# Performance work log

Hardware: AMD Instinct MI355X
Metric: run time of the kernel (lower is better)

Reference implementation:

```python
import jax, jax.numpy as jnp
import numpy as np

INPUT_DIM = 512
DEGREE = 3
NUM_KNOTS = 16
NUM_NEURONS = 1024
OUTPUT_DIM = 512
NUM_BASIS = NUM_KNOTS + DEGREE - 1  # 18


def make_knots():
    # uniform grid on [0,1], extended by `degree` knots on each side
    h = 1.0 / (NUM_KNOTS - 1)
    grid = np.linspace(0.0, 1.0, NUM_KNOTS)
    lo = grid[0] - h * np.arange(DEGREE, 0, -1)
    hi = grid[-1] + h * np.arange(1, DEGREE + 1)
    return jnp.asarray(np.concatenate([lo, grid, hi]), dtype=jnp.float32)  # [NUM_KNOTS+2*DEGREE]


def bspline_basis(x, t, degree):
    # x: [B, N]; t: [K] uniform extended knots. Cox-de Boor recursion.
    K = t.shape[0]
    xb = x[..., None]
    B = ((xb >= t[:-1]) & (xb < t[1:])).astype(x.dtype)  # [B, N, K-1]
    for p in range(1, degree + 1):
        ti = t[: K - p - 1]
        tip = t[p : K - 1]
        ti1 = t[1 : K - p]
        tip1 = t[p + 1 : K]
        left = (xb - ti) / (tip - ti) * B[..., :-1]
        right = (tip1 - xb) / (tip1 - ti1) * B[..., 1:]
        B = left + right
    return B  # [B, N, K-1-degree] == [B, N, NUM_BASIS]


def norm_layer(x, eps=1e-8):
    # per-row min-max normalization into the spline domain [0,1)
    mn = jnp.min(x, axis=-1, keepdims=True)
    mx = jnp.max(x, axis=-1, keepdims=True)
    return (x - mn) / (mx - mn + eps)


def setup_inputs() -> dict:
    key = jax.random.key(0)
    ks = jax.random.split(key, 7)
    x = jax.random.normal(ks[0], (4096, INPUT_DIM), dtype=jnp.float32)
    s1 = 1.0 / np.sqrt(INPUT_DIM)
    s2 = 1.0 / np.sqrt(NUM_NEURONS)
    W1 = jax.random.uniform(ks[1], (INPUT_DIM, NUM_NEURONS), jnp.float32, -s1, s1)
    b1 = jax.random.uniform(ks[2], (NUM_NEURONS,), jnp.float32, -s1, s1)
    coeff = jax.random.normal(ks[3], (NUM_NEURONS, NUM_BASIS), dtype=jnp.float32) * 0.1
    sp_bias = jnp.zeros((NUM_NEURONS,), dtype=jnp.float32)
    W2 = jax.random.uniform(ks[4], (NUM_NEURONS, OUTPUT_DIM), jnp.float32, -s2, s2)
    b2 = jax.random.uniform(ks[5], (OUTPUT_DIM,), jnp.float32, -s2, s2)
    return {"x": x, "W1": W1, "b1": b1, "coeff": coeff, "sp_bias": sp_bias, "W2": W2, "b2": b2}


def reference(x, W1, b1, coeff, sp_bias, W2, b2):
    t = make_knots()
    h = x @ W1 + b1                      # [B, N]  Linear 1
    h = norm_layer(h)                    # NormLayer -> [0,1)
    basis = bspline_basis(h, t, DEGREE)  # [B, N, NUM_BASIS]
    sp = jnp.einsum('bnk,nk->bn', basis, coeff) + sp_bias  # per-neuron spline eval
    out = sp @ W2 + b2                   # Linear 2
    return jax.nn.relu(out)
```

## Files before the change

### kernel.cpp

```cpp
#include <hip/hip_runtime.h>

#define M_ROWS  4096
#define IN_DIM  512
#define NEURONS 1024
#define OUT_DIM 512

typedef _Float16 f16;
typedef __attribute__((ext_vector_type(8))) _Float16 f16x8;
typedef __attribute__((ext_vector_type(4))) _Float16 f16x4;
typedef __attribute__((ext_vector_type(4))) float    f32x4;

__global__ __launch_bounds__(256) void prep(
    const float* __restrict__ x,  f16* __restrict__ xh,
    const float* __restrict__ W1, f16* __restrict__ W1t,
    const float* __restrict__ W2, f16* __restrict__ W2t,
    const float* __restrict__ coeff, const float* __restrict__ spb,
    float* __restrict__ cp)
{
    __shared__ float S[32][33];
    const int b = blockIdx.x, t = threadIdx.x;
    if (b < 1024) {
        int i = b * 256 + t;
        const float4* p = (const float4*)x;
        float4 a = p[i * 2], c = p[i * 2 + 1];
        f16x8 o = { (f16)a.x, (f16)a.y, (f16)a.z, (f16)a.w,
                    (f16)c.x, (f16)c.y, (f16)c.z, (f16)c.w };
        *(f16x8*)(xh + (size_t)i * 8) = o;
        return;
    }
    if (b < 1536) {
        const int tile = b - 1024;
        const int tx = tile & 31, ty = tile >> 5;
        const int tr = t >> 3, tc = (t & 7) * 4;
        float4 v = *(const float4*)&W1[(size_t)(ty * 32 + tr) * NEURONS + tx * 32 + tc];
        S[tr][tc + 0] = v.x; S[tr][tc + 1] = v.y;
        S[tr][tc + 2] = v.z; S[tr][tc + 3] = v.w;
        __syncthreads();
        f16x4 o = {(f16)S[tc + 0][tr], (f16)S[tc + 1][tr],
                   (f16)S[tc + 2][tr], (f16)S[tc + 3][tr]};
        *(f16x4*)&W1t[(size_t)(tx * 32 + tr) * IN_DIM + ty * 32 + tc] = o;
        return;
    }
    if (b < 2048) {
        const int tile = b - 1536;
        const int nt = tile & 15, kt2 = tile >> 4;
        const int tr = t >> 3, tc = (t & 7) * 4;
        float4 v = *(const float4*)&W2[(size_t)(kt2 * 32 + tr) * OUT_DIM + nt * 32 + tc];
        S[tr][tc + 0] = v.x; S[tr][tc + 1] = v.y;
        S[tr][tc + 2] = v.z; S[tr][tc + 3] = v.w;
        __syncthreads();
        f16x4 o = {(f16)S[tc + 0][tr], (f16)S[tc + 1][tr],
                   (f16)S[tc + 2][tr], (f16)S[tc + 3][tr]};
        *(f16x4*)&W2t[(size_t)(nt * 32 + tr) * NEURONS + kt2 * 32 + tc] = o;
        return;
    }
    {
        const int tid = (b - 2048) * 256 + t;
        if (tid < NEURONS * 15) {
            const int n = tid / 15, ii = tid % 15;
            const float s = spb[n];
            float4 c;
            c.x = coeff[n * 18 + ii]     + s;
            c.y = coeff[n * 18 + ii + 1] + s;
            c.z = coeff[n * 18 + ii + 2] + s;
            c.w = coeff[n * 18 + ii + 3] + s;
            *(float4*)&cp[(size_t)tid * 4] = c;
        }
    }
}

__global__ __launch_bounds__(256) void k_gemm1(
    const f16* __restrict__ A, const f16* __restrict__ Bt,
    const float* __restrict__ b1, f16* __restrict__ h,
    float* __restrict__ pmin, float* __restrict__ pmax)
{
    __shared__ f16 lds[2][(128 + 64) * 64];

    const int t    = threadIdx.x;
    const int lane = t & 63, l15 = lane & 15, lhi = lane >> 4;
    const int wid  = t >> 6;
    const int wm   = wid >> 1, wn = wid & 1;

    const int flat = blockIdx.y * gridDim.x + blockIdx.x;
    const int swz  = (flat & 7) * 64 + (flat >> 3);
    const int m0   = (swz >> 4) * 128;
    const int n0   = (swz & 15) * 64;

    auto stage = [&](int buf, int kt) {
        f16* base = &lds[buf][0];
#pragma unroll
        for (int j = 0; j < 4; ++j) {
            int c = wid * 4 + j;
            const f16* g = A + (size_t)(m0 + c * 8 + (lane >> 3)) * IN_DIM + kt + (lane & 7) * 8;
            __builtin_amdgcn_global_load_lds(
                (const __attribute__((address_space(1))) void*)g,
                (__attribute__((address_space(3))) void*)(base + c * 512), 16, 0, 0);
        }
#pragma unroll
        for (int j = 0; j < 2; ++j) {
            int c = wid * 2 + j;
            const f16* g = Bt + (size_t)(n0 + c * 8 + (lane >> 3)) * IN_DIM + kt + (lane & 7) * 8;
            __builtin_amdgcn_global_load_lds(
                (const __attribute__((address_space(1))) void*)g,
                (__attribute__((address_space(3))) void*)(base + 8192 + c * 512), 16, 0, 0);
        }
    };

    f32x4 acc[4][2];
#pragma unroll
    for (int i = 0; i < 4; ++i)
#pragma unroll
        for (int j = 0; j < 2; ++j) acc[i][j] = (f32x4)0.f;

    stage(0, 0);
    __syncthreads();

    int cur = 0;
    for (int tt = 0; tt < 8; ++tt) {
        if (tt < 7) stage(cur ^ 1, (tt + 1) * 64);
        const f16* L = &lds[cur][0];
#pragma unroll
        for (int ks = 0; ks < 2; ++ks) {
            f16x8 bfr[2];
#pragma unroll
            for (int nj = 0; nj < 2; ++nj)
                bfr[nj] = *(const f16x8*)
                    &L[8192 + (wn * 32 + nj * 16 + l15) * 64 + ks * 32 + lhi * 8];
#pragma unroll
            for (int mi = 0; mi < 4; ++mi) {
                f16x8 afr = *(const f16x8*)
                    &L[(wm * 64 + mi * 16 + l15) * 64 + ks * 32 + lhi * 8];
#pragma unroll
                for (int nj = 0; nj < 2; ++nj)
                    acc[mi][nj] = __builtin_amdgcn_mfma_f32_16x16x32_f16(
                        afr, bfr[nj], acc[mi][nj], 0, 0, 0);
            }
        }
        __syncthreads();
        cur ^= 1;
    }

    const int nb2 = (n0 >> 6) * 2 + wn;
#pragma unroll
    for (int mi = 0; mi < 4; ++mi) {
        const int row0 = m0 + wm * 64 + mi * 16 + lhi * 4;
        float vmn[4], vmx[4];
#pragma unroll
        for (int nj = 0; nj < 2; ++nj) {
            const int col = n0 + wn * 32 + nj * 16 + l15;
            const float bv = b1[col];
#pragma unroll
            for (int j = 0; j < 4; ++j) {
                f16 hv = (f16)(acc[mi][nj][j] + bv);
                h[(size_t)(row0 + j) * NEURONS + col] = hv;
                float vr = (float)hv;
                if (nj == 0) { vmn[j] = vr; vmx[j] = vr; }
                else { vmn[j] = fminf(vmn[j], vr); vmx[j] = fmaxf(vmx[j], vr); }
            }
        }
#pragma unroll
        for (int j = 0; j < 4; ++j) {
#pragma unroll
            for (int d = 1; d < 16; d <<= 1) {
                vmn[j] = fminf(vmn[j], __shfl_xor(vmn[j], d));
                vmx[j] = fmaxf(vmx[j], __shfl_xor(vmx[j], d));
            }
        }
        if (l15 == 0) {
#pragma unroll
            for (int j = 0; j < 4; ++j) {
                pmin[(size_t)nb2 * M_ROWS + row0 + j] = vmn[j];
                pmax[(size_t)nb2 * M_ROWS + row0 + j] = vmx[j];
            }
        }
    }
}

__global__ __launch_bounds__(256) void k_spline(
    const f16* __restrict__ h, const float* __restrict__ pmin,
    const float* __restrict__ pmax, const float* __restrict__ cp,
    f16* __restrict__ sph)
{
    const int t    = threadIdx.x;
    const int lane = t & 63;
    const int row  = blockIdx.x * 4 + (t >> 6);

    float mn = pmin[(size_t)(lane & 31) * M_ROWS + row];
    float mx = pmax[(size_t)(lane & 31) * M_ROWS + row];
#pragma unroll
    for (int d = 1; d < 32; d <<= 1) {
        mn = fminf(mn, __shfl_xor(mn, d));
        mx = fmaxf(mx, __shfl_xor(mx, d));
    }
    const float inv = 1.0f / (mx - mn + 1e-8f);

#pragma unroll
    for (int half = 0; half < 2; ++half) {
        const int k0 = half * 512 + lane * 8;
        f16x8 hv = *(const f16x8*)&h[(size_t)row * NEURONS + k0];
        f16x8 o;
#pragma unroll
        for (int e = 0; e < 8; ++e) {
            const float u   = ((float)hv[e] - mn) * inv;
            const float t15 = u * 15.0f;
            int ii = (int)t15;
            ii = ii < 0 ? 0 : (ii > 14 ? 14 : ii);
            const float tl  = t15 - (float)ii;
            const float t2  = tl * tl, t3 = t2 * tl;
            const float omt = 1.0f - tl;
            const float b0  = omt * omt * omt * (1.0f / 6.0f);
            const float b3v = t3 * (1.0f / 6.0f);
            const float b1v = (4.0f / 6.0f) - t2 + 0.5f * t3;
            const float b2v = (1.0f / 6.0f) + 0.5f * (tl + t2 - t3);
            const float4 c  = *(const float4*)&cp[((size_t)(k0 + e) * 15 + ii) * 4];
            o[e] = (f16)(c.x * b0 + c.y * b1v + c.z * b2v + c.w * b3v);
        }
        *(f16x8*)&sph[(size_t)row * NEURONS + k0] = o;
    }
}

__global__ __launch_bounds__(256) void k_gemm2(
    const f16* __restrict__ A, const f16* __restrict__ Bt,
    const float* __restrict__ b2, float* __restrict__ out)
{
    __shared__ f16 lds[2][128 * 128];

    const int t    = threadIdx.x;
    const int lane = t & 63, l15 = lane & 15, lhi = lane >> 4;
    const int wid  = t >> 6;
    const int wm   = wid >> 1, wn = wid & 1;

    const int flat = blockIdx.x;
    const int swz  = (flat & 7) * 64 + (flat >> 3);
    const int m0   = (swz >> 3) * 64;
    const int n0   = (swz & 7) * 64;

    auto stage = [&](int buf, int kt) {
        f16* base = &lds[buf][0];
#pragma unroll
        for (int j = 0; j < 4; ++j) {
            int c = wid * 4 + j;
            const f16* g = A + (size_t)(m0 + c * 4 + (lane >> 4)) * NEURONS + kt + (lane & 15) * 8;
            __builtin_amdgcn_global_load_lds(
                (const __attribute__((address_space(1))) void*)g,
                (__attribute__((address_space(3))) void*)(base + c * 512), 16, 0, 0);
        }
#pragma unroll
        for (int j = 0; j < 4; ++j) {
            int c = wid * 4 + j;
            const f16* g = Bt + (size_t)(n0 + c * 4 + (lane >> 4)) * NEURONS + kt + (lane & 15) * 8;
            __builtin_amdgcn_global_load_lds(
                (const __attribute__((address_space(1))) void*)g,
                (__attribute__((address_space(3))) void*)(base + 8192 + c * 512), 16, 0, 0);
        }
    };

    f32x4 acc[2][2];
#pragma unroll
    for (int i = 0; i < 2; ++i)
#pragma unroll
        for (int j = 0; j < 2; ++j) acc[i][j] = (f32x4)0.f;

    stage(0, 0);
    __syncthreads();

    int cur = 0;
    for (int tt = 0; tt < 8; ++tt) {
        if (tt < 7) stage(cur ^ 1, (tt + 1) * 128);
        const f16* L = &lds[cur][0];
#pragma unroll
        for (int ks = 0; ks < 4; ++ks) {
            f16x8 bfr[2];
#pragma unroll
            for (int nj = 0; nj < 2; ++nj)
                bfr[nj] = *(const f16x8*)
                    &L[8192 + (wn * 32 + nj * 16 + l15) * 128 + ks * 32 + lhi * 8];
#pragma unroll
            for (int mi = 0; mi < 2; ++mi) {
                f16x8 afr = *(const f16x8*)
                    &L[(wm * 32 + mi * 16 + l15) * 128 + ks * 32 + lhi * 8];
#pragma unroll
                for (int nj = 0; nj < 2; ++nj)
                    acc[mi][nj] = __builtin_amdgcn_mfma_f32_16x16x32_f16(
                        afr, bfr[nj], acc[mi][nj], 0, 0, 0);
            }
        }
        __syncthreads();
        cur ^= 1;
    }

#pragma unroll
    for (int mi = 0; mi < 2; ++mi) {
        const int row0 = m0 + wm * 32 + mi * 16 + lhi * 4;
#pragma unroll
        for (int nj = 0; nj < 2; ++nj) {
            const int col = n0 + wn * 32 + nj * 16 + l15;
            const float bv = b2[col];
#pragma unroll
            for (int j = 0; j < 4; ++j)
                out[(size_t)(row0 + j) * OUT_DIM + col] =
                    fmaxf(acc[mi][nj][j] + bv, 0.0f);
        }
    }
}

extern "C" void kernel_launch(void* const* d_in, const int* in_sizes, int n_in,
                              void* d_out, int out_size, void* d_ws, size_t ws_size,
                              hipStream_t stream)
{
    const float* x     = (const float*)d_in[0];
    const float* W1    = (const float*)d_in[1];
    const float* b1    = (const float*)d_in[2];
    const float* coeff = (const float*)d_in[3];
    const float* spb   = (const float*)d_in[4];
    const float* W2    = (const float*)d_in[5];
    const float* b2    = (const float*)d_in[6];
    float* out = (float*)d_out;

    char* ws = (char*)d_ws;
    f16*   h    = (f16*)ws;
    f16*   sph  = (f16*)(ws + ( 8u << 20));
    f16*   xh   = (f16*)(ws + (16u << 20));
    f16*   W1t  = (f16*)(ws + (20u << 20));
    f16*   W2t  = (f16*)(ws + (21u << 20));
    float* pmin = (float*)(ws + (22u << 20));
    float* pmax = (float*)(ws + (22u << 20) + (512u << 10));
    float* cp   = (float*)(ws + (23u << 20));

    prep<<<dim3(2108), 256, 0, stream>>>(x, xh, W1, W1t, W2, W2t, coeff, spb, cp);

    k_gemm1<<<dim3(16, 32), 256, 0, stream>>>(xh, W1t, b1, h, pmin, pmax);

    k_spline<<<dim3(1024), 256, 0, stream>>>(h, pmin, pmax, cp, sph);

    k_gemm2<<<dim3(512), 256, 0, stream>>>(sph, W2t, b2, out);
}
```

Measured before the change: 53.80 us.

## Fuse spline evaluation into second GEMM as the A-operand producer

Removes the standalone spline kernel and the sph intermediate buffer. The second GEMM now computes spline values on the fly from h into LDS for each 64-wide K tile, while W2 tiles are still streamed with direct global-to-LDS loads. Output tiles grow to 64x128 on a 256-block grid, and the per-row min/max reduction is done per block. Spline coefficients are also stored in fp16 to halve gather traffic. The risks are that spline math is recomputed by every N-tile (4x redundancy), the grid gives only about one block per CU, and coefficient precision drops.

```diff
diff --git a/kernel.cpp b/kernel.cpp
--- a/kernel.cpp
+++ b/kernel.cpp
@@ -15,7 +15,7 @@
     const float* __restrict__ W1, f16* __restrict__ W1t,
     const float* __restrict__ W2, f16* __restrict__ W2t,
     const float* __restrict__ coeff, const float* __restrict__ spb,
-    float* __restrict__ cp)
+    f16* __restrict__ cpH)
 {
     __shared__ float S[32][33];
     const int b = blockIdx.x, t = threadIdx.x;
@@ -59,12 +59,12 @@
         if (tid < NEURONS * 15) {
             const int n = tid / 15, ii = tid % 15;
             const float s = spb[n];
-            float4 c;
-            c.x = coeff[n * 18 + ii]     + s;
-            c.y = coeff[n * 18 + ii + 1] + s;
-            c.z = coeff[n * 18 + ii + 2] + s;
-            c.w = coeff[n * 18 + ii + 3] + s;
-            *(float4*)&cp[(size_t)tid * 4] = c;
+            f16x4 c;
+            c[0] = (f16)(coeff[n * 18 + ii]     + s);
+            c[1] = (f16)(coeff[n * 18 + ii + 1] + s);
+            c[2] = (f16)(coeff[n * 18 + ii + 2] + s);
+            c[3] = (f16)(coeff[n * 18 + ii + 3] + s);
+            *(f16x4*)&cpH[(size_t)tid * 4] = c;
         }
     }
 }
@@ -176,54 +176,15 @@
     }
 }
 
-__global__ __launch_bounds__(256) void k_spline(
+__global__ __launch_bounds__(256) void sp_gemm2(
     const f16* __restrict__ h, const float* __restrict__ pmin,
-    const float* __restrict__ pmax, const float* __restrict__ cp,
-    f16* __restrict__ sph)
+    const float* __restrict__ pmax, const f16* __restrict__ cpH,
+    const f16* __restrict__ W2t, const float* __restrict__ b2,
+    float* __restrict__ out)
 {
-    const int t    = threadIdx.x;
-    const int lane = t & 63;
-    const int row  = blockIdx.x * 4 + (t >> 6);
-
-    float mn = pmin[(size_t)(lane & 31) * M_ROWS + row];
-    float mx = pmax[(size_t)(lane & 31) * M_ROWS + row];
-#pragma unroll
-    for (int d = 1; d < 32; d <<= 1) {
-        mn = fminf(mn, __shfl_xor(mn, d));
-        mx = fmaxf(mx, __shfl_xor(mx, d));
-    }
-    const float inv = 1.0f / (mx - mn + 1e-8f);
-
-#pragma unroll
-    for (int half = 0; half < 2; ++half) {
-        const int k0 = half * 512 + lane * 8;
-        f16x8 hv = *(const f16x8*)&h[(size_t)row * NEURONS + k0];
-        f16x8 o;
-#pragma unroll
-        for (int e = 0; e < 8; ++e) {
-            const float u   = ((float)hv[e] - mn) * inv;
-            const float t15 = u * 15.0f;
-            int ii = (int)t15;
-            ii = ii < 0 ? 0 : (ii > 14 ? 14 : ii);
-            const float tl  = t15 - (float)ii;
-            const float t2  = tl * tl, t3 = t2 * tl;
-            const float omt = 1.0f - tl;
-            const float b0  = omt * omt * omt * (1.0f / 6.0f);
-            const float b3v = t3 * (1.0f / 6.0f);
-            const float b1v = (4.0f / 6.0f) - t2 + 0.5f * t3;
-            const float b2v = (1.0f / 6.0f) + 0.5f * (tl + t2 - t3);
-            const float4 c  = *(const float4*)&cp[((size_t)(k0 + e) * 15 + ii) * 4];
-            o[e] = (f16)(c.x * b0 + c.y * b1v + c.z * b2v + c.w * b3v);
-        }
-        *(f16x8*)&sph[(size_t)row * NEURONS + k0] = o;
-    }
-}
-
-__global__ __launch_bounds__(256) void k_gemm2(
-    const f16* __restrict__ A, const f16* __restrict__ Bt,
-    const float* __restrict__ b2, float* __restrict__ out)
-{
-    __shared__ f16 lds[2][128 * 128];
+    __shared__ __align__(16) f16 Bb[2][128 * 64];
+    __shared__ __align__(16) f16 Aa[2][64 * 72];
+    __shared__ float mnS[64], invS[64];
 
     const int t    = threadIdx.x;
     const int lane = t & 63, l15 = lane & 15, lhi = lane >> 4;
@@ -231,56 +192,94 @@
     const int wm   = wid >> 1, wn = wid & 1;
 
     const int flat = blockIdx.x;
-    const int swz  = (flat & 7) * 64 + (flat >> 3);
-    const int m0   = (swz >> 3) * 64;
-    const int n0   = (swz & 7) * 64;
-
-    auto stage = [&](int buf, int kt) {
-        f16* base = &lds[buf][0];
+    const int swz  = (flat & 7) * 32 + (flat >> 3);
+    const int m0   = (swz & 63) * 64;
+    const int n0   = (swz >> 6) * 128;
+
+    auto stageB = [&](int bf, int tt) {
+        f16* base = &Bb[bf][0];
 #pragma unroll
         for (int j = 0; j < 4; ++j) {
-            int c = wid * 4 + j;
-            const f16* g = A + (size_t)(m0 + c * 4 + (lane >> 4)) * NEURONS + kt + (lane & 15) * 8;
+            const int c = wid * 4 + j;
+            const f16* src = W2t + (size_t)(n0 + c * 8 + (lane >> 3)) * NEURONS
+                             + tt * 64 + (lane & 7) * 8;
             __builtin_amdgcn_global_load_lds(
-                (const __attribute__((address_space(1))) void*)g,
+                (const __attribute__((address_space(1))) void*)src,
                 (__attribute__((address_space(3))) void*)(base + c * 512), 16, 0, 0);
         }
-#pragma unroll
-        for (int j = 0; j < 4; ++j) {
-            int c = wid * 4 + j;
-            const f16* g = Bt + (size_t)(n0 + c * 4 + (lane >> 4)) * NEURONS + kt + (lane & 15) * 8;
-            __builtin_amdgcn_global_load_lds(
-                (const __attribute__((address_space(1))) void*)g,
-                (__attribute__((address_space(3))) void*)(base + 8192 + c * 512), 16, 0, 0);
-        }
     };
 
-    f32x4 acc[2][2];
+    auto splineA = [&](int bf, int tt) {
+        const int r_  = t & 63;
+        const int sg  = (t >> 6) * 16;
+        const float mn = mnS[r_], inv = invS[r_];
+#pragma unroll
+        for (int hf = 0; hf < 2; ++hf) {
+            const int kg = tt * 64 + sg + hf * 8;
+            f16x8 hv = *(const f16x8*)&h[(size_t)(m0 + r_) * NEURONS + kg];
+            f16x8 o;
+#pragma unroll
+            for (int e = 0; e < 8; ++e) {
+                const float u   = ((float)hv[e] - mn) * inv;
+                const float t15 = u * 15.0f;
+                int ii = (int)t15;
+                ii = ii < 0 ? 0 : (ii > 14 ? 14 : ii);
+                const float tl  = t15 - (float)ii;
+                const float t2  = tl * tl, t3 = t2 * tl;
+                const float omt = 1.0f - tl;
+                const float b0  = omt * omt * omt * (1.0f / 6.0f);
+                const float b3v = t3 * (1.0f / 6.0f);
+                const float b1v = (4.0f / 6.0f) - t2 + 0.5f * t3;
+                const float b2v = (1.0f / 6.0f) + 0.5f * (tl + t2 - t3);
+                const f16x4 c   = *(const f16x4*)&cpH[((size_t)(kg + e) * 15 + ii) * 4];
+                o[e] = (f16)((float)c[0] * b0 + (float)c[1] * b1v
+                           + (float)c[2] * b2v + (float)c[3] * b3v);
+            }
+            *(f16x8*)&Aa[bf][r_ * 72 + sg + hf * 8] = o;
+        }
+    };
+
+    stageB(0, 0);
+    if (t < 64) {
+        const int row = m0 + t;
+        float a = pmin[row], b = pmax[row];
+#pragma unroll
+        for (int p = 1; p < 32; ++p) {
+            a = fminf(a, pmin[(size_t)p * M_ROWS + row]);
+            b = fmaxf(b, pmax[(size_t)p * M_ROWS + row]);
+        }
+        mnS[t] = a;
+        invS[t] = 1.0f / (b - a + 1e-8f);
+    }
+    __syncthreads();
+    splineA(0, 0);
+    __syncthreads();
+
+    f32x4 acc[2][4];
 #pragma unroll
     for (int i = 0; i < 2; ++i)
 #pragma unroll
-        for (int j = 0; j < 2; ++j) acc[i][j] = (f32x4)0.f;
-
-    stage(0, 0);
-    __syncthreads();
+        for (int j = 0; j < 4; ++j) acc[i][j] = (f32x4)0.f;
 
     int cur = 0;
-    for (int tt = 0; tt < 8; ++tt) {
-        if (tt < 7) stage(cur ^ 1, (tt + 1) * 128);
-        const f16* L = &lds[cur][0];
-#pragma unroll
-        for (int ks = 0; ks < 4; ++ks) {
-            f16x8 bfr[2];
-#pragma unroll
-            for (int nj = 0; nj < 2; ++nj)
+    for (int tt = 0; tt < 16; ++tt) {
+        if (tt < 15) {
+            stageB(cur ^ 1, tt + 1);
+            splineA(cur ^ 1, tt + 1);
+        }
+#pragma unroll
+        for (int ks = 0; ks < 2; ++ks) {
+            f16x8 bfr[4];
+#pragma unroll
+            for (int nj = 0; nj < 4; ++nj)
                 bfr[nj] = *(const f16x8*)
-                    &L[8192 + (wn * 32 + nj * 16 + l15) * 128 + ks * 32 + lhi * 8];
+                    &Bb[cur][(wn * 64 + nj * 16 + l15) * 64 + ks * 32 + lhi * 8];
 #pragma unroll
             for (int mi = 0; mi < 2; ++mi) {
                 f16x8 afr = *(const f16x8*)
-                    &L[(wm * 32 + mi * 16 + l15) * 128 + ks * 32 + lhi * 8];
-#pragma unroll
-                for (int nj = 0; nj < 2; ++nj)
+                    &Aa[cur][(wm * 32 + mi * 16 + l15) * 72 + ks * 32 + lhi * 8];
+#pragma unroll
+                for (int nj = 0; nj < 4; ++nj)
                     acc[mi][nj] = __builtin_amdgcn_mfma_f32_16x16x32_f16(
                         afr, bfr[nj], acc[mi][nj], 0, 0, 0);
             }
@@ -293,8 +292,8 @@
     for (int mi = 0; mi < 2; ++mi) {
         const int row0 = m0 + wm * 32 + mi * 16 + lhi * 4;
 #pragma unroll
-        for (int nj = 0; nj < 2; ++nj) {
-            const int col = n0 + wn * 32 + nj * 16 + l15;
+        for (int nj = 0; nj < 4; ++nj) {
+            const int col = n0 + wn * 64 + nj * 16 + l15;
             const float bv = b2[col];
 #pragma unroll
             for (int j = 0; j < 4; ++j)
@@ -319,19 +318,16 @@
 
     char* ws = (char*)d_ws;
     f16*   h    = (f16*)ws;
-    f16*   sph  = (f16*)(ws + ( 8u << 20));
-    f16*   xh   = (f16*)(ws + (16u << 20));
-    f16*   W1t  = (f16*)(ws + (20u << 20));
-    f16*   W2t  = (f16*)(ws + (21u << 20));
-    float* pmin = (float*)(ws + (22u << 20));
-    float* pmax = (float*)(ws + (22u << 20) + (512u << 10));
-    float* cp   = (float*)(ws + (23u << 20));
-
-    prep<<<dim3(2108), 256, 0, stream>>>(x, xh, W1, W1t, W2, W2t, coeff, spb, cp);
+    f16*   xh   = (f16*)(ws + ( 8u << 20));
+    f16*   W1t  = (f16*)(ws + (12u << 20));
+    f16*   W2t  = (f16*)(ws + (13u << 20));
+    float* pmin = (float*)(ws + (14u << 20));
+    float* pmax = (float*)(ws + (14u << 20) + (512u << 10));
+    f16*   cpH  = (f16*)(ws + (15u << 20));
+
+    prep<<<dim3(2108), 256, 0, stream>>>(x, xh, W1, W1t, W2, W2t, coeff, spb, cpH);
 
     k_gemm1<<<dim3(16, 32), 256, 0, stream>>>(xh, W1t, b1, h, pmin, pmax);
 
-    k_spline<<<dim3(1024), 256, 0, stream>>>(h, pmin, pmax, cp, sph);
-
-    k_gemm2<<<dim3(512), 256, 0, stream>>>(sph, W2t, b2, out);
+    sp_gemm2<<<dim3(256), 256, 0, stream>>>(h, pmin, pmax, cpH, W2t, b2, out);
 }
```

New measurement: 84.70 us. 57.4% more time.

## Precompute fp16 cubic polynomial coefficients and XOR-swizzle gemm2 operand layouts

Applied to the files above, without the earlier changes.

The spline stage now reads per-interval polynomial coefficients in fp16 instead of four fp32 control points. It evaluates the cubic with Horner's rule, which cuts the gather bandwidth in half and removes the basis-weight arithmetic. Separately, the spline output and the transposed W2 are stored with a 16-byte XOR swizzle keyed on row, and gemm2's LDS fragment reads apply the same swizzle to reduce bank conflicts. Storing the coefficients in fp16 lowers precision slightly, and the swizzle has to match exactly between producers and consumer.

```diff
diff --git a/kernel.cpp b/kernel.cpp
--- a/kernel.cpp
+++ b/kernel.cpp
@@ -15,7 +15,7 @@
     const float* __restrict__ W1, f16* __restrict__ W1t,
     const float* __restrict__ W2, f16* __restrict__ W2t,
     const float* __restrict__ coeff, const float* __restrict__ spb,
-    float* __restrict__ cp)
+    f16* __restrict__ qH)
 {
     __shared__ float S[32][33];
     const int b = blockIdx.x, t = threadIdx.x;
@@ -49,9 +49,11 @@
         S[tr][tc + 0] = v.x; S[tr][tc + 1] = v.y;
         S[tr][tc + 2] = v.z; S[tr][tc + 3] = v.w;
         __syncthreads();
+        const int n = nt * 32 + tr;
         f16x4 o = {(f16)S[tc + 0][tr], (f16)S[tc + 1][tr],
                    (f16)S[tc + 2][tr], (f16)S[tc + 3][tr]};
-        *(f16x4*)&W2t[(size_t)(nt * 32 + tr) * NEURONS + kt2 * 32 + tc] = o;
+        const int kbyte = ((kt2 * 32 + tc) * 2) ^ ((n & 3) << 4);
+        *(f16x4*)((char*)W2t + (size_t)n * 2048 + kbyte) = o;
         return;
     }
     {
@@ -59,12 +61,16 @@
         if (tid < NEURONS * 15) {
             const int n = tid / 15, ii = tid % 15;
             const float s = spb[n];
-            float4 c;
-            c.x = coeff[n * 18 + ii]     + s;
-            c.y = coeff[n * 18 + ii + 1] + s;
-            c.z = coeff[n * 18 + ii + 2] + s;
-            c.w = coeff[n * 18 + ii + 3] + s;
-            *(float4*)&cp[(size_t)tid * 4] = c;
+            const float c0 = coeff[n * 18 + ii]     + s;
+            const float c1 = coeff[n * 18 + ii + 1] + s;
+            const float c2 = coeff[n * 18 + ii + 2] + s;
+            const float c3 = coeff[n * 18 + ii + 3] + s;
+            f16x4 q;
+            q[0] = (f16)((c0 + 4.0f * c1 + c2) * (1.0f / 6.0f));
+            q[1] = (f16)((c2 - c0) * 0.5f);
+            q[2] = (f16)((c0 - 2.0f * c1 + c2) * 0.5f);
+            q[3] = (f16)((c3 - c0 + 3.0f * (c1 - c2)) * (1.0f / 6.0f));
+            *(f16x4*)&qH[(size_t)tid * 4] = q;
         }
     }
 }
@@ -178,7 +184,7 @@
 
 __global__ __launch_bounds__(256) void k_spline(
     const f16* __restrict__ h, const float* __restrict__ pmin,
-    const float* __restrict__ pmax, const float* __restrict__ cp,
+    const float* __restrict__ pmax, const f16* __restrict__ qH,
     f16* __restrict__ sph)
 {
     const int t    = threadIdx.x;
@@ -192,7 +198,9 @@
         mn = fminf(mn, __shfl_xor(mn, d));
         mx = fmaxf(mx, __shfl_xor(mx, d));
     }
-    const float inv = 1.0f / (mx - mn + 1e-8f);
+    const float s15 = 15.0f / (mx - mn + 1e-8f);
+    const float o15 = -mn * s15;
+    const int   swz = (row & 3) << 4;
 
 #pragma unroll
     for (int half = 0; half < 2; ++half) {
@@ -201,21 +209,17 @@
         f16x8 o;
 #pragma unroll
         for (int e = 0; e < 8; ++e) {
-            const float u   = ((float)hv[e] - mn) * inv;
-            const float t15 = u * 15.0f;
-            int ii = (int)t15;
-            ii = ii < 0 ? 0 : (ii > 14 ? 14 : ii);
-            const float tl  = t15 - (float)ii;
-            const float t2  = tl * tl, t3 = t2 * tl;
-            const float omt = 1.0f - tl;
-            const float b0  = omt * omt * omt * (1.0f / 6.0f);
-            const float b3v = t3 * (1.0f / 6.0f);
-            const float b1v = (4.0f / 6.0f) - t2 + 0.5f * t3;
-            const float b2v = (1.0f / 6.0f) + 0.5f * (tl + t2 - t3);
-            const float4 c  = *(const float4*)&cp[((size_t)(k0 + e) * 15 + ii) * 4];
-            o[e] = (f16)(c.x * b0 + c.y * b1v + c.z * b2v + c.w * b3v);
-        }
-        *(f16x8*)&sph[(size_t)row * NEURONS + k0] = o;
+            const float t15 = fmaf((float)hv[e], s15, o15);
+            float fi = floorf(t15);
+            fi = fminf(fmaxf(fi, 0.0f), 14.0f);
+            const int   ii = (int)fi;
+            const float tl = t15 - fi;
+            const f16x4 q  = *(const f16x4*)&qH[((size_t)(k0 + e) * 15 + ii) * 4];
+            o[e] = (f16)fmaf(fmaf(fmaf((float)q[3], tl, (float)q[2]),
+                                  tl, (float)q[1]),
+                             tl, (float)q[0]);
+        }
+        *(f16x8*)((char*)sph + (size_t)row * 2048 + ((k0 * 2) ^ swz)) = o;
     }
 }
 
@@ -264,21 +268,24 @@
     stage(0, 0);
     __syncthreads();
 
+    const int sA = (l15 & 3) << 4;
     int cur = 0;
     for (int tt = 0; tt < 8; ++tt) {
         if (tt < 7) stage(cur ^ 1, (tt + 1) * 128);
-        const f16* L = &lds[cur][0];
+        const char* L = (const char*)&lds[cur][0];
 #pragma unroll
         for (int ks = 0; ks < 4; ++ks) {
+            const int ko = (ks * 64 + lhi * 16) ^ sA;
             f16x8 bfr[2];
 #pragma unroll
-            for (int nj = 0; nj < 2; ++nj)
-                bfr[nj] = *(const f16x8*)
-                    &L[8192 + (wn * 32 + nj * 16 + l15) * 128 + ks * 32 + lhi * 8];
+            for (int nj = 0; nj < 2; ++nj) {
+                const int cl = wn * 32 + nj * 16 + l15;
+                bfr[nj] = *(const f16x8*)(L + 16384 + (size_t)cl * 256 + ko);
+            }
 #pragma unroll
             for (int mi = 0; mi < 2; ++mi) {
-                f16x8 afr = *(const f16x8*)
-                    &L[(wm * 32 + mi * 16 + l15) * 128 + ks * 32 + lhi * 8];
+                const int ar = wm * 32 + mi * 16 + l15;
+                f16x8 afr = *(const f16x8*)(L + (size_t)ar * 256 + ko);
 #pragma unroll
                 for (int nj = 0; nj < 2; ++nj)
                     acc[mi][nj] = __builtin_amdgcn_mfma_f32_16x16x32_f16(
@@ -325,13 +332,13 @@
     f16*   W2t  = (f16*)(ws + (21u << 20));
     float* pmin = (float*)(ws + (22u << 20));
     float* pmax = (float*)(ws + (22u << 20) + (512u << 10));
-    float* cp   = (float*)(ws + (23u << 20));
-
-    prep<<<dim3(2108), 256, 0, stream>>>(x, xh, W1, W1t, W2, W2t, coeff, spb, cp);
+    f16*   qH   = (f16*)(ws + (23u << 20));
+
+    prep<<<dim3(2108), 256, 0, stream>>>(x, xh, W1, W1t, W2, W2t, coeff, spb, qH);
 
     k_gemm1<<<dim3(16, 32), 256, 0, stream>>>(xh, W1t, b1, h, pmin, pmax);
 
-    k_spline<<<dim3(1024), 256, 0, stream>>>(h, pmin, pmax, cp, sph);
+    k_spline<<<dim3(1024), 256, 0, stream>>>(h, pmin, pmax, qH, sph);
 
     k_gemm2<<<dim3(512), 256, 0, stream>>>(sph, W2t, b2, out);
 }
```

Result: faster. 51.02 us (-5.2%).
